# Optimization experiments

Hardware: AMD Instinct MI355X
Metric: run time of the kernel (lower is better)

## Reference

```python
import jax, jax.numpy as jnp
import numpy as np

D = 128      # embedding dim
T = 8        # message passing rounds (config.training.T)
NV = 4000    # n_vars
NL = 2 * NV  # n_literals
NC = 16000   # n_clauses


def setup_inputs() -> dict:
    key = jax.random.key(0)
    ks = jax.random.split(key, 12)
    s = np.float32(1.0 / np.sqrt(D))
    return {
        "L_state": jax.random.normal(ks[0], (1, NL, D), jnp.float32),
        "C_state": jax.random.normal(ks[1], (1, NC, D), jnp.float32),
        "hidden_L": jnp.zeros((1, NL, D), jnp.float32),
        "hidden_C": jnp.zeros((1, NC, D), jnp.float32),
        # 0/1 literal-clause incidence, ~40 clauses per literal
        "M": (jax.random.uniform(ks[2], (NL, NC)) < 0.0025).astype(jnp.float32),
        "n_vars": NV,
        "W_lc": jax.random.normal(ks[3], (D, D), jnp.float32) * s,
        "b_lc": jnp.zeros((D,), jnp.float32),
        "W_cl": jax.random.normal(ks[4], (D, D), jnp.float32) * s,
        "b_cl": jnp.zeros((D,), jnp.float32),
        "Wih_C": jax.random.normal(ks[5], (4 * D, D), jnp.float32) * s,
        "Whh_C": jax.random.normal(ks[6], (4 * D, D), jnp.float32) * s,
        "bih_C": jnp.zeros((4 * D,), jnp.float32),
        "bhh_C": jnp.zeros((4 * D,), jnp.float32),
        "Wih_L": jax.random.normal(ks[7], (4 * D, 2 * D), jnp.float32) * s,
        "Whh_L": jax.random.normal(ks[8], (4 * D, D), jnp.float32) * s,
        "bih_L": jnp.zeros((4 * D,), jnp.float32),
        "bhh_L": jnp.zeros((4 * D,), jnp.float32),
    }


def lstm_cell(x, h, c, Wih, Whh, bih, bhh):
    # torch nn.LSTM gate order: i, f, g, o
    gates = x @ Wih.T + bih + h @ Whh.T + bhh
    i, f, g, o = jnp.split(gates, 4, axis=-1)
    c_new = jax.nn.sigmoid(f) * c + jax.nn.sigmoid(i) * jnp.tanh(g)
    h_new = jax.nn.sigmoid(o) * jnp.tanh(c_new)
    return h_new, c_new


def reference(L_state, C_state, hidden_L, hidden_C, M, n_vars,
              W_lc, b_lc, W_cl, b_cl,
              Wih_C, Whh_C, bih_C, bhh_C,
              Wih_L, Whh_L, bih_L, bhh_L):
    # Replicates torch flip() as written: slices dim 0 (size 1), so this is
    # effectively identity for n_vars >= 1 (first slice is empty, second is x).
    def flip(x):
        return jnp.concatenate([x[n_vars:2 * n_vars], x[0:n_vars]], axis=0)

    def step(carry, _):
        L, hL, hC = carry
        LC_pre = L @ W_lc.T + b_lc                        # (1, NL, D)
        LC_msgs = jnp.einsum('lc,sld->scd', M, LC_pre)    # M^T @ pre: (1, NC, D)
        Cs, hC = lstm_cell(LC_msgs, hC, hC, Wih_C, Whh_C, bih_C, bhh_C)
        CL_pre = Cs @ W_cl.T + b_cl                       # (1, NC, D)
        CL_msgs = jnp.einsum('lc,scd->sld', M, CL_pre)    # M @ pre: (1, NL, D)
        inp = jnp.concatenate([CL_msgs, flip(L)], axis=2) # (1, NL, 2D)
        L, hL = lstm_cell(inp, hL, hL, Wih_L, Whh_L, bih_L, bhh_L)
        return (L, hL, hC), None

    (L_final, _, _), _ = jax.lax.scan(step, (L_state, hidden_L, hidden_C), None, length=T)
    return L_final
```

## Files before the change

### kernel.cpp

```cpp
#include <hip/hip_runtime.h>

#define DD   128
#define NL   8000
#define NC   16000
#define TSTEPS 8
#define NBF  2
#define ROWW 96
#define COLW 64

#define OS   33
#define SPLITS8 (32 * OS)
#define SPLIT   (SPLITS8 * 8)
#define LSTR 17
#define LSPL (48 * LSTR * 8)
#define L2S  33
#define L2SPL (48 * L2S * 8)

typedef __attribute__((ext_vector_type(8))) short  short8;
typedef __attribute__((ext_vector_type(8))) _Float16 half8;
typedef __attribute__((ext_vector_type(4))) float  f32x4;

__device__ __forceinline__ float frcp(float x) { return __builtin_amdgcn_rcpf(x); }
__device__ __forceinline__ float sigm(float x) { return frcp(1.f + __expf(-x)); }
__device__ __forceinline__ float tanh_(float x) {
  float e = __expf(2.f * x);
  return 1.f - 2.f * frcp(e + 1.f);
}
__device__ __forceinline__ void add4(float4& a, const float4 b) {
  a.x += b.x; a.y += b.y; a.z += b.z; a.w += b.w;
}
__device__ __forceinline__ unsigned short bfround(float v) {
  unsigned u = __float_as_uint(v);
  return (unsigned short)((u + 0x7FFF + ((u >> 16) & 1)) >> 16);
}
__device__ __forceinline__ float bf2f(unsigned short b) {
  return __uint_as_float(((unsigned)b) << 16);
}
__device__ __forceinline__ void splitf16(float v, unsigned short& h, unsigned short& l) {
  _Float16 hh = (_Float16)v;
  float r = v - (float)hh;
  _Float16 ll = (_Float16)r;
  h = __builtin_bit_cast(unsigned short, hh);
  l = __builtin_bit_cast(unsigned short, ll);
}
__device__ __forceinline__ int4 packi4(const unsigned short* p) {
  return make_int4(p[0] | ((int)p[1] << 16), p[2] | ((int)p[3] << 16),
                   p[4] | ((int)p[5] << 16), p[6] | ((int)p[7] << 16));
}

__device__ __forceinline__ void store_oct3(unsigned short* A, int oct, int m,
                                           float4 a, float4 b) {
  float f[8] = {a.x, a.y, a.z, a.w, b.x, b.y, b.z, b.w};
  unsigned short h[8], md[8], lo[8];
  #pragma unroll
  for (int j = 0; j < 8; ++j) {
    h[j] = bfround(f[j]);
    float r1 = f[j] - bf2f(h[j]);
    md[j] = bfround(r1);
    float r2 = r1 - bf2f(md[j]);
    lo[j] = bfround(r2);
  }
  int base = (oct * OS + m) * 8;
  *(int4*)(A + base)             = packi4(h);
  *(int4*)(A + SPLIT + base)     = packi4(md);
  *(int4*)(A + 2 * SPLIT + base) = packi4(lo);
}

__device__ __forceinline__ void store_oct2g(unsigned short* A, int strideS8, int plane,
                                            int oct, int m, float4 a, float4 b) {
  float f[8] = {a.x, a.y, a.z, a.w, b.x, b.y, b.z, b.w};
  unsigned short h[8], lo[8];
  #pragma unroll
  for (int j = 0; j < 8; ++j) splitf16(f[j], h[j], lo[j]);
  int base = (oct * strideS8 + m) * 8;
  *(int4*)(A + base)         = packi4(h);
  *(int4*)(A + plane + base) = packi4(lo);
}

__device__ __forceinline__ void store_half3L(unsigned short* A, int oct, int half, int m,
                                             float4 a) {
  float f[4] = {a.x, a.y, a.z, a.w};
  unsigned short h[4], md[4], lo[4];
  #pragma unroll
  for (int j = 0; j < 4; ++j) {
    h[j] = bfround(f[j]);
    float r1 = f[j] - bf2f(h[j]);
    md[j] = bfround(r1);
    float r2 = r1 - bf2f(md[j]);
    lo[j] = bfround(r2);
  }
  int base = (oct * LSTR + m) * 8 + half * 4;
  *(int2*)(A + base)            = make_int2(h[0]  | ((int)h[1]  << 16), h[2]  | ((int)h[3]  << 16));
  *(int2*)(A + LSPL + base)     = make_int2(md[0] | ((int)md[1] << 16), md[2] | ((int)md[3] << 16));
  *(int2*)(A + 2 * LSPL + base) = make_int2(lo[0] | ((int)lo[1] << 16), lo[2] | ((int)lo[3] << 16));
}

#define MFMA6(ACC, AH, AM, AL, BH, BM, BL)                                   \
  ACC = __builtin_amdgcn_mfma_f32_16x16x32_bf16(AH, BH, ACC, 0, 0, 0);       \
  ACC = __builtin_amdgcn_mfma_f32_16x16x32_bf16(AH, BM, ACC, 0, 0, 0);       \
  ACC = __builtin_amdgcn_mfma_f32_16x16x32_bf16(AM, BH, ACC, 0, 0, 0);       \
  ACC = __builtin_amdgcn_mfma_f32_16x16x32_bf16(AH, BL, ACC, 0, 0, 0);       \
  ACC = __builtin_amdgcn_mfma_f32_16x16x32_bf16(AL, BH, ACC, 0, 0, 0);       \
  ACC = __builtin_amdgcn_mfma_f32_16x16x32_bf16(AM, BM, ACC, 0, 0, 0);

#define MFMA4(ACC, AH, AL, BH, BL)                                           \
  ACC = __builtin_amdgcn_mfma_f32_16x16x32_f16(AH, BH, ACC, 0, 0, 0);        \
  ACC = __builtin_amdgcn_mfma_f32_16x16x32_f16(AH, BL, ACC, 0, 0, 0);        \
  ACC = __builtin_amdgcn_mfma_f32_16x16x32_f16(AL, BH, ACC, 0, 0, 0);        \
  ACC = __builtin_amdgcn_mfma_f32_16x16x32_f16(AL, BL, ACC, 0, 0, 0);


__global__ __launch_bounds__(256) void init_states(
    float4* __restrict__ Lbuf, const float4* __restrict__ L0,
    float4* __restrict__ hL, const float4* __restrict__ hL0,
    float4* __restrict__ hC, const float4* __restrict__ hC0) {
  int i = blockIdx.x * 256 + threadIdx.x, stride = gridDim.x * 256;
  for (int j = i; j < NL * DD / 4; j += stride) { Lbuf[j] = L0[j]; hL[j] = hL0[j]; }
  for (int j = i; j < NC * DD / 4; j += stride) hC[j] = hC0[j];
}

__global__ __launch_bounds__(256) void scan_M(const float4* __restrict__ M4,
                                              int* __restrict__ csr, int* __restrict__ csc,
                                              int* __restrict__ rcnt, int* __restrict__ ccnt) {
  const int total = (NL * NC) / 4;
  int stride = gridDim.x * blockDim.x;
  for (int i = blockIdx.x * blockDim.x + threadIdx.x; i < total; i += stride) {
    float4 v = M4[i];
    if (v.x == 0.f && v.y == 0.f && v.z == 0.f && v.w == 0.f) continue;
    int base = i * 4;
    int l = base / NC;
    int c0 = base - l * NC;
    float vv[4] = {v.x, v.y, v.z, v.w};
    #pragma unroll
    for (int e = 0; e < 4; ++e) {
      if (vv[e] != 0.f) {
        int c = c0 + e;
        int rp = atomicAdd(&rcnt[l], 1);
        if (rp < ROWW) csr[l * ROWW + rp] = c;
        int cp = atomicAdd(&ccnt[c], 1);
        if (cp < COLW) csc[c * COLW + cp] = l;
      }
    }
  }
}

__device__ __forceinline__ void split_store_bf3(float w, int idx, unsigned short* hi,
                                                unsigned short* md, unsigned short* lo) {
  unsigned short h = bfround(w);
  float r1 = w - bf2f(h);
  unsigned short m = bfround(r1);
  float r2 = r1 - bf2f(m);
  hi[idx] = h; md[idx] = m; lo[idx] = bfround(r2);
}

__global__ __launch_bounds__(256) void build_packC(
    const float* __restrict__ WihC, const float* __restrict__ Wlc, const float* __restrict__ WhhC,
    unsigned short* __restrict__ pkhi, unsigned short* __restrict__ pkmd, unsigned short* __restrict__ pklo,
    unsigned short* __restrict__ qkhi, unsigned short* __restrict__ qklo) {
  int i = blockIdx.x * 256 + threadIdx.x;
  int k = i >> 9, n = i & 511;
  float w;
  if (k < 128) {
    float s = 0.f;
    for (int d = 0; d < 128; ++d) s += WihC[n * 128 + d] * Wlc[d * 128 + k];
    w = s;
  } else {
    w = WhhC[n * 128 + (k - 128)];
  }
  int idx = ((k >> 3) * 512 + n) * 8 + (k & 7);
  split_store_bf3(w, idx, pkhi, pkmd, pklo);
  splitf16(w, qkhi[idx], qklo[idx]);
}

__global__ __launch_bounds__(256) void build_packL(
    const float* __restrict__ WihL, const float* __restrict__ Wcl, const float* __restrict__ WhhL,
    unsigned short* __restrict__ pkhi, unsigned short* __restrict__ pkmd, unsigned short* __restrict__ pklo,
    unsigned short* __restrict__ qkhi, unsigned short* __restrict__ qklo) {
  int i = blockIdx.x * 256 + threadIdx.x;
  int k = i >> 9, n = i & 511;
  float w;
  if (k < 128) {
    float s = 0.f;
    for (int d = 0; d < 128; ++d) s += WihL[n * 256 + d] * Wcl[d * 128 + k];
    w = s;
  } else if (k < 256) {
    w = WihL[n * 256 + k];
  } else {
    w = WhhL[n * 128 + (k - 256)];
  }
  int idx = ((k >> 3) * 512 + n) * 8 + (k & 7);
  split_store_bf3(w, idx, pkhi, pkmd, pklo);
  splitf16(w, qkhi[idx], qklo[idx]);
}

__global__ __launch_bounds__(256) void build_bias(
    const float* __restrict__ bihC, const float* __restrict__ bhhC,
    const float* __restrict__ WihC, const float* __restrict__ blc,
    const float* __restrict__ bihL, const float* __restrict__ bhhL,
    const float* __restrict__ WihL, const float* __restrict__ bcl,
    float* __restrict__ bsumC, float* __restrict__ bvecC,
    float* __restrict__ bsumL, float* __restrict__ bvecL) {
  int i = blockIdx.x * 256 + threadIdx.x;
  if (i < 512) {
    bsumC[i] = bihC[i] + bhhC[i];
    float s = 0.f;
    for (int d = 0; d < 128; ++d) s += WihC[i * 128 + d] * blc[d];
    bvecC[i] = s;
  } else if (i < 1024) {
    int n = i - 512;
    bsumL[n] = bihL[n] + bhhL[n];
    float s = 0.f;
    for (int d = 0; d < 128; ++d) s += WihL[n * 256 + d] * bcl[d];
    bvecL[n] = s;
  }
}

__device__ __forceinline__ void clause_epilogue(
    const f32x4 acc[2][4], const float* bsum, const float* bvec, const int* ccnt,
    float* hC, float* Cs, int rowBase, int quad, int cw) {
  float bs_[4], bv_[4];
  #pragma unroll
  for (int g = 0; g < 4; ++g) { bs_[g] = bsum[g * 128 + cw]; bv_[g] = bvec[g * 128 + cw]; }
  #pragma unroll
  for (int mt = 0; mt < 2; ++mt) {
    #pragma unroll
    for (int reg = 0; reg < 4; ++reg) {
      int row = rowBase + mt * 16 + quad * 4 + reg;
      float deg = (float)ccnt[row];
      float co = hC[(size_t)row * DD + cw];
      float iv = acc[mt][0][reg] + bs_[0] + deg * bv_[0];
      float fv = acc[mt][1][reg] + bs_[1] + deg * bv_[1];
      float gv = acc[mt][2][reg] + bs_[2] + deg * bv_[2];
      float ov = acc[mt][3][reg] + bs_[3] + deg * bv_[3];
      float cn = sigm(fv) * co + sigm(iv) * tanh_(gv);
      hC[(size_t)row * DD + cw] = cn;
      Cs[(size_t)row * DD + cw] = sigm(ov) * tanh_(cn);
    }
  }
}

__device__ __forceinline__ void literal_epilogue2(
    const f32x4 acc[2][4], const float* bsum, const float* bvec, const int* rcnt,
    float* hL, float* Lbuf, int rowBase, int quad, int cw) {
  float bs_[4], bv_[4];
  #pragma unroll
  for (int g = 0; g < 4; ++g) { bs_[g] = bsum[g * 128 + cw]; bv_[g] = bvec[g * 128 + cw]; }
  #pragma unroll
  for (int mt = 0; mt < 2; ++mt) {
    #pragma unroll
    for (int reg = 0; reg < 4; ++reg) {
      int row = rowBase + mt * 16 + quad * 4 + reg;
      float deg = (float)rcnt[row];
      float co = hL[(size_t)row * DD + cw];
      float iv = acc[mt][0][reg] + bs_[0] + deg * bv_[0];
      float fv = acc[mt][1][reg] + bs_[1] + deg * bv_[1];
      float gv = acc[mt][2][reg] + bs_[2] + deg * bv_[2];
      float ov = acc[mt][3][reg] + bs_[3] + deg * bv_[3];
      float cn = sigm(fv) * co + sigm(iv) * tanh_(gv);
      hL[(size_t)row * DD + cw] = cn;
      Lbuf[(size_t)row * DD + cw] = sigm(ov) * tanh_(cn);
    }
  }
}


template <int NOCT, bool STAGE_H>
__global__ __launch_bounds__(512, 4) void clause_bf3(
    const float* __restrict__ Lbuf, const int* __restrict__ csc, const int* __restrict__ ccnt,
    const unsigned short* __restrict__ pkhi, const unsigned short* __restrict__ pkmd,
    const unsigned short* __restrict__ pklo,
    const float* __restrict__ bsum, const float* __restrict__ bvec,
    float* __restrict__ hC, float* __restrict__ Cs) {
  __shared__ unsigned short A[3 * SPLIT];
  __shared__ int IDX[32 * COLW];
  const int t = threadIdx.x;
  const int rowBase = blockIdx.x * 32;

  ((int4*)IDX)[t] = ((const int4*)(csc + rowBase * COLW))[t];
  __syncthreads();

  {
    const int r = t >> 4, sub = t & 15;
    const int c = rowBase + r;
    int cnt = ccnt[c]; if (cnt > COLW) cnt = COLW;
    const int* lst = IDX + r * COLW;
    float4 a0 = make_float4(0, 0, 0, 0), a1 = a0;
    int j = 0;
    for (; j + 8 <= cnt; j += 8) {
      float4 p0[8], p1[8];
      #pragma unroll
      for (int u = 0; u < 8; ++u) {
        const float4* s4 = (const float4*)(Lbuf + (size_t)lst[j + u] * DD) + sub * 2;
        p0[u] = s4[0]; p1[u] = s4[1];
      }
      #pragma unroll
      for (int u = 0; u < 8; ++u) { add4(a0, p0[u]); add4(a1, p1[u]); }
    }
    for (; j < cnt; ++j) {
      const float4* s4 = (const float4*)(Lbuf + (size_t)lst[j] * DD) + sub * 2;
      add4(a0, s4[0]); add4(a1, s4[1]);
    }
    store_oct3(A, sub, r, a0, a1);
    if constexpr (STAGE_H) {
      const float4* h4 = (const float4*)(hC + (size_t)c * DD) + sub * 2;
      store_oct3(A, 16 + sub, r, h4[0], h4[1]);
    }
  }
  __syncthreads();

  const int w = t >> 6, l = t & 63;
  const int quad = l >> 4, lane16 = l & 15;
  const int cw = w * 16 + lane16;
  f32x4 acc[2][4];
  #pragma unroll
  for (int mt = 0; mt < 2; ++mt)
    #pragma unroll
    for (int g = 0; g < 4; ++g) acc[mt][g] = (f32x4){0.f, 0.f, 0.f, 0.f};

  const short8* As = (const short8*)A;
  const short8* Bh = (const short8*)pkhi;
  const short8* Bm = (const short8*)pkmd;
  const short8* Bl = (const short8*)pklo;

  __builtin_amdgcn_s_setprio(1);
  #pragma unroll
  for (int s = 0; s < NOCT / 4; ++s) {
    int ao = (s * 4 + quad) * OS + lane16;
    short8 a0h = As[ao],                a1h = As[ao + 16];
    short8 a0m = As[SPLITS8 + ao],      a1m = As[SPLITS8 + ao + 16];
    short8 a0l = As[2 * SPLITS8 + ao],  a1l = As[2 * SPLITS8 + ao + 16];
    int bo = (s * 4 + quad) * 512 + cw;
    #pragma unroll
    for (int g = 0; g < 4; ++g) {
      short8 bh = Bh[bo + g * 128];
      short8 bm = Bm[bo + g * 128];
      short8 bl = Bl[bo + g * 128];
      MFMA6(acc[0][g], a0h, a0m, a0l, bh, bm, bl);
      MFMA6(acc[1][g], a1h, a1m, a1l, bh, bm, bl);
    }
  }
  __builtin_amdgcn_s_setprio(0);
  clause_epilogue(acc, bsum, bvec, ccnt, hC, Cs, rowBase, quad, cw);
}

template <int NOCT, bool STAGE_H>
__global__ __launch_bounds__(512, 4) void literal_bf3(
    const float* __restrict__ Cs, const int* __restrict__ csr, const int* __restrict__ rcnt,
    const unsigned short* __restrict__ pkhi, const unsigned short* __restrict__ pkmd,
    const unsigned short* __restrict__ pklo,
    const float* __restrict__ bsum, const float* __restrict__ bvec,
    float* __restrict__ hL, float* __restrict__ Lbuf) {
  __shared__ unsigned short A[3 * LSPL];
  __shared__ int IDX[16 * ROWW];
  const int t = threadIdx.x;
  const int rowBase = blockIdx.x * 16;

  if (t < 384) ((int4*)IDX)[t] = ((const int4*)(csr + rowBase * ROWW))[t];
  __syncthreads();

  {
    const int r = t >> 5, cg2 = t & 31;
    const int lr = rowBase + r;
    int cnt = rcnt[lr]; if (cnt > ROWW) cnt = ROWW;
    const int* lst = IDX + r * ROWW;
    float4 a0 = make_float4(0, 0, 0, 0);
    int j = 0;
    for (; j + 8 <= cnt; j += 8) {
      float4 p[8];
      #pragma unroll
      for (int u = 0; u < 8; ++u)
        p[u] = ((const float4*)(Cs + (size_t)lst[j + u] * DD))[cg2];
      #pragma unroll
      for (int u = 0; u < 8; ++u) add4(a0, p[u]);
    }
    for (; j < cnt; ++j)
      add4(a0, ((const float4*)(Cs + (size_t)lst[j] * DD))[cg2]);
    store_half3L(A, cg2 >> 1, cg2 & 1, r, a0);
    store_half3L(A, 16 + (cg2 >> 1), cg2 & 1, r,
                 ((const float4*)(Lbuf + (size_t)lr * DD))[cg2]);
    if constexpr (STAGE_H)
      store_half3L(A, 32 + (cg2 >> 1), cg2 & 1, r,
                   ((const float4*)(hL + (size_t)lr * DD))[cg2]);
  }
  __syncthreads();

  const int w = t >> 6, l = t & 63;
  const int quad = l >> 4, lane16 = l & 15;
  const int cw = w * 16 + lane16;
  f32x4 acc[4];
  #pragma unroll
  for (int g = 0; g < 4; ++g) acc[g] = (f32x4){0.f, 0.f, 0.f, 0.f};

  const short8* As = (const short8*)A;
  const short8* Bh = (const short8*)pkhi;
  const short8* Bm = (const short8*)pkmd;
  const short8* Bl = (const short8*)pklo;

  __builtin_amdgcn_s_setprio(1);
  #pragma unroll
  for (int s = 0; s < NOCT / 4; ++s) {
    int ao = (s * 4 + quad) * LSTR + lane16;
    short8 ah = As[ao];
    short8 am = As[LSPL / 8 + ao];
    short8 al = As[2 * (LSPL / 8) + ao];
    int bo = (s * 4 + quad) * 512 + cw;
    #pragma unroll
    for (int g = 0; g < 4; ++g) {
      short8 bh = Bh[bo + g * 128];
      short8 bm = Bm[bo + g * 128];
      short8 bl = Bl[bo + g * 128];
      MFMA6(acc[g], ah, am, al, bh, bm, bl);
    }
  }
  __builtin_amdgcn_s_setprio(0);

  float bs_[4], bv_[4];
  #pragma unroll
  for (int g = 0; g < 4; ++g) { bs_[g] = bsum[g * 128 + cw]; bv_[g] = bvec[g * 128 + cw]; }
  #pragma unroll
  for (int reg = 0; reg < 4; ++reg) {
    int row = rowBase + quad * 4 + reg;
    float deg = (float)rcnt[row];
    float co = hL[(size_t)row * DD + cw];
    float iv = acc[0][reg] + bs_[0] + deg * bv_[0];
    float fv = acc[1][reg] + bs_[1] + deg * bv_[1];
    float gv = acc[2][reg] + bs_[2] + deg * bv_[2];
    float ov = acc[3][reg] + bs_[3] + deg * bv_[3];
    float cn = sigm(fv) * co + sigm(iv) * tanh_(gv);
    hL[(size_t)row * DD + cw] = cn;
    Lbuf[(size_t)row * DD + cw] = sigm(ov) * tanh_(cn);
  }
}


__global__ __launch_bounds__(512, 4) void clause_f2(
    const float* __restrict__ Lbuf, const int* __restrict__ csc, const int* __restrict__ ccnt,
    const unsigned short* __restrict__ qkhi, const unsigned short* __restrict__ qklo,
    const float* __restrict__ bsum, const float* __restrict__ bvec,
    float* __restrict__ hC, float* __restrict__ Cs) {
  __shared__ unsigned short A[2 * SPLIT];
  __shared__ int IDX[32 * COLW];
  const int t = threadIdx.x;
  const int rowBase = blockIdx.x * 32;

  ((int4*)IDX)[t] = ((const int4*)(csc + rowBase * COLW))[t];
  __syncthreads();

  {
    const int r = t >> 4, sub = t & 15;
    const int c = rowBase + r;
    int cnt = ccnt[c]; if (cnt > COLW) cnt = COLW;
    const int* lst = IDX + r * COLW;
    float4 a0 = make_float4(0, 0, 0, 0), a1 = a0;
    int j = 0;
    for (; j + 8 <= cnt; j += 8) {
      float4 p0[8], p1[8];
      #pragma unroll
      for (int u = 0; u < 8; ++u) {
        const float4* s4 = (const float4*)(Lbuf + (size_t)lst[j + u] * DD) + sub * 2;
        p0[u] = s4[0]; p1[u] = s4[1];
      }
      #pragma unroll
      for (int u = 0; u < 8; ++u) { add4(a0, p0[u]); add4(a1, p1[u]); }
    }
    for (; j < cnt; ++j) {
      const float4* s4 = (const float4*)(Lbuf + (size_t)lst[j] * DD) + sub * 2;
      add4(a0, s4[0]); add4(a1, s4[1]);
    }
    store_oct2g(A, OS, SPLIT, sub, r, a0, a1);
    const float4* h4 = (const float4*)(hC + (size_t)c * DD) + sub * 2;
    store_oct2g(A, OS, SPLIT, 16 + sub, r, h4[0], h4[1]);
  }
  __syncthreads();

  const int w = t >> 6, l = t & 63;
  const int quad = l >> 4, lane16 = l & 15;
  const int cw = w * 16 + lane16;
  f32x4 acc[2][4];
  #pragma unroll
  for (int mt = 0; mt < 2; ++mt)
    #pragma unroll
    for (int g = 0; g < 4; ++g) acc[mt][g] = (f32x4){0.f, 0.f, 0.f, 0.f};

  const half8* As = (const half8*)A;
  const half8* Bh = (const half8*)qkhi;
  const half8* Bl = (const half8*)qklo;

  __builtin_amdgcn_s_setprio(1);
  #pragma unroll
  for (int s = 0; s < 8; ++s) {
    int ao = (s * 4 + quad) * OS + lane16;
    half8 a0h = As[ao],           a1h = As[ao + 16];
    half8 a0l = As[SPLITS8 + ao], a1l = As[SPLITS8 + ao + 16];
    int bo = (s * 4 + quad) * 512 + cw;
    #pragma unroll
    for (int g = 0; g < 4; ++g) {
      half8 bh = Bh[bo + g * 128];
      half8 bl = Bl[bo + g * 128];
      MFMA4(acc[0][g], a0h, a0l, bh, bl);
      MFMA4(acc[1][g], a1h, a1l, bh, bl);
    }
  }
  __builtin_amdgcn_s_setprio(0);
  clause_epilogue(acc, bsum, bvec, ccnt, hC, Cs, rowBase, quad, cw);
}

__global__ __launch_bounds__(512, 4) void literal_f2(
    const float* __restrict__ Cs, const int* __restrict__ csr, const int* __restrict__ rcnt,
    const unsigned short* __restrict__ qkhi, const unsigned short* __restrict__ qklo,
    const float* __restrict__ bsum, const float* __restrict__ bvec,
    float* __restrict__ hL, float* __restrict__ Lbuf) {
  __shared__ unsigned short A[2 * L2SPL];
  __shared__ int IDX[32 * ROWW];
  const int t = threadIdx.x;
  const int rowBase = blockIdx.x * 32;

  ((int4*)IDX)[t] = ((const int4*)(csr + rowBase * ROWW))[t];
  if (t < 256) ((int4*)IDX)[t + 512] = ((const int4*)(csr + rowBase * ROWW))[t + 512];
  __syncthreads();

  {
    const int r = t >> 4, sub = t & 15;
    const int lr = rowBase + r;
    int cnt = rcnt[lr]; if (cnt > ROWW) cnt = ROWW;
    const int* lst = IDX + r * ROWW;
    float4 a0 = make_float4(0, 0, 0, 0), a1 = a0;
    int j = 0;
    for (; j + 8 <= cnt; j += 8) {
      float4 p0[8], p1[8];
      #pragma unroll
      for (int u = 0; u < 8; ++u) {
        const float4* s4 = (const float4*)(Cs + (size_t)lst[j + u] * DD) + sub * 2;
        p0[u] = s4[0]; p1[u] = s4[1];
      }
      #pragma unroll
      for (int u = 0; u < 8; ++u) { add4(a0, p0[u]); add4(a1, p1[u]); }
    }
    for (; j < cnt; ++j) {
      const float4* s4 = (const float4*)(Cs + (size_t)lst[j] * DD) + sub * 2;
      add4(a0, s4[0]); add4(a1, s4[1]);
    }
    store_oct2g(A, L2S, L2SPL, sub, r, a0, a1);
    const float4* l4 = (const float4*)(Lbuf + (size_t)lr * DD) + sub * 2;
    store_oct2g(A, L2S, L2SPL, 16 + sub, r, l4[0], l4[1]);
    const float4* h4 = (const float4*)(hL + (size_t)lr * DD) + sub * 2;
    store_oct2g(A, L2S, L2SPL, 32 + sub, r, h4[0], h4[1]);
  }
  __syncthreads();

  const int w = t >> 6, l = t & 63;
  const int quad = l >> 4, lane16 = l & 15;
  const int cw = w * 16 + lane16;
  f32x4 acc[2][4];
  #pragma unroll
  for (int mt = 0; mt < 2; ++mt)
    #pragma unroll
    for (int g = 0; g < 4; ++g) acc[mt][g] = (f32x4){0.f, 0.f, 0.f, 0.f};

  const half8* As = (const half8*)A;
  const half8* Bh = (const half8*)qkhi;
  const half8* Bl = (const half8*)qklo;

  __builtin_amdgcn_s_setprio(1);
  #pragma unroll
  for (int s = 0; s < 12; ++s) {
    int ao = (s * 4 + quad) * L2S + lane16;
    half8 a0h = As[ao],             a1h = As[ao + 16];
    half8 a0l = As[L2SPL / 8 + ao], a1l = As[L2SPL / 8 + ao + 16];
    int bo = (s * 4 + quad) * 512 + cw;
    #pragma unroll
    for (int g = 0; g < 4; ++g) {
      half8 bh = Bh[bo + g * 128];
      half8 bl = Bl[bo + g * 128];
      MFMA4(acc[0][g], a0h, a0l, bh, bl);
      MFMA4(acc[1][g], a1h, a1l, bh, bl);
    }
  }
  __builtin_amdgcn_s_setprio(0);
  literal_epilogue2(acc, bsum, bvec, rcnt, hL, Lbuf, rowBase, quad, cw);
}


extern "C" void kernel_launch(void* const* d_in, const int* in_sizes, int n_in,
                              void* d_out, int out_size, void* d_ws, size_t ws_size,
                              hipStream_t stream) {
  const float* L0   = (const float*)d_in[0];
  const float* hL0  = (const float*)d_in[2];
  const float* hC0  = (const float*)d_in[3];
  const float* M    = (const float*)d_in[4];
  const float* Wlc  = (const float*)d_in[6];
  const float* blc  = (const float*)d_in[7];
  const float* Wcl  = (const float*)d_in[8];
  const float* bcl  = (const float*)d_in[9];
  const float* WihC = (const float*)d_in[10];
  const float* WhhC = (const float*)d_in[11];
  const float* bihC = (const float*)d_in[12];
  const float* bhhC = (const float*)d_in[13];
  const float* WihL = (const float*)d_in[14];
  const float* WhhL = (const float*)d_in[15];
  const float* bihL = (const float*)d_in[16];
  const float* bhhL = (const float*)d_in[17];

  float* ws    = (float*)d_ws;
  float* hL    = ws;
  float* hC    = hL + NL * DD;
  float* Cs    = hC + NC * DD;
  float* bsumC = Cs + NC * DD;
  float* bvecC = bsumC + 512;
  float* bsumL = bvecC + 512;
  float* bvecL = bsumL + 512;
  unsigned short* pkChi = (unsigned short*)(bvecL + 512);
  unsigned short* pkCmd = pkChi + 256 * 512;
  unsigned short* pkClo = pkCmd + 256 * 512;
  unsigned short* pkLhi = pkClo + 256 * 512;
  unsigned short* pkLmd = pkLhi + 384 * 512;
  unsigned short* pkLlo = pkLmd + 384 * 512;
  unsigned short* qkChi = pkLlo + 384 * 512;
  unsigned short* qkClo = qkChi + 256 * 512;
  unsigned short* qkLhi = qkClo + 256 * 512;
  unsigned short* qkLlo = qkLhi + 384 * 512;
  int* csr  = (int*)(qkLlo + 384 * 512);
  int* csc  = csr + NL * ROWW;
  int* rcnt = csc + NC * COLW;
  int* ccnt = rcnt + NL;
  float* Lbuf = (float*)d_out;

  hipMemsetAsync(rcnt, 0, (NL + NC) * sizeof(int), stream);

  init_states<<<1024, 256, 0, stream>>>((float4*)Lbuf, (const float4*)L0,
                                        (float4*)hL, (const float4*)hL0,
                                        (float4*)hC, (const float4*)hC0);

  scan_M<<<4096, 256, 0, stream>>>((const float4*)M, csr, csc, rcnt, ccnt);

  build_packC<<<(256 * 512) / 256, 256, 0, stream>>>(WihC, Wlc, WhhC,
                                                     pkChi, pkCmd, pkClo, qkChi, qkClo);
  build_packL<<<(384 * 512) / 256, 256, 0, stream>>>(WihL, Wcl, WhhL,
                                                     pkLhi, pkLmd, pkLlo, qkLhi, qkLlo);
  build_bias<<<4, 256, 0, stream>>>(bihC, bhhC, WihC, blc, bihL, bhhL, WihL, bcl,
                                    bsumC, bvecC, bsumL, bvecL);

  clause_bf3<16, false><<<NC / 32, 512, 0, stream>>>(Lbuf, csc, ccnt, pkChi, pkCmd, pkClo,
                                                     bsumC, bvecC, hC, Cs);
  literal_bf3<32, false><<<NL / 16, 512, 0, stream>>>(Cs, csr, rcnt, pkLhi, pkLmd, pkLlo,
                                                      bsumL, bvecL, hL, Lbuf);
  for (int t = 1; t < NBF; ++t) {
    clause_bf3<32, true><<<NC / 32, 512, 0, stream>>>(Lbuf, csc, ccnt, pkChi, pkCmd, pkClo,
                                                      bsumC, bvecC, hC, Cs);
    literal_bf3<48, true><<<NL / 16, 512, 0, stream>>>(Cs, csr, rcnt, pkLhi, pkLmd, pkLlo,
                                                       bsumL, bvecL, hL, Lbuf);
  }
  for (int t = NBF; t < TSTEPS; ++t) {
    clause_f2<<<NC / 32, 512, 0, stream>>>(Lbuf, csc, ccnt, qkChi, qkClo,
                                           bsumC, bvecC, hC, Cs);
    literal_f2<<<NL / 32, 512, 0, stream>>>(Cs, csr, rcnt, qkLhi, qkLlo,
                                            bsumL, bvecL, hL, Lbuf);
  }
}
```

Measured before the change: 1.280 ms.

## Shrink all step kernels to 16-row, 256-thread blocks with 8 column tiles per wave

Every clause and literal kernel now handles 16 rows per block with 4 waves instead of 32 rows with 8 waves. Each wave covers two 64-column halves, giving 8 accumulator tiles per gate set. The shared-memory A layout uses a single stride of 17, and the literal bf3 kernel drops its shared index staging and reads CSR indices straight from global memory. The aim is more, smaller blocks for better occupancy and load balance across CUs on the gather-heavy phases. The cost is loading the B weights once per 16 rows instead of once per 32, which doubles weight traffic per output row.

```diff
diff --git a/kernel.cpp b/kernel.cpp
--- a/kernel.cpp
+++ b/kernel.cpp
@@ -8,13 +8,9 @@
 #define ROWW 96
 #define COLW 64
 
-#define OS   33
-#define SPLITS8 (32 * OS)
-#define SPLIT   (SPLITS8 * 8)
-#define LSTR 17
-#define LSPL (48 * LSTR * 8)
-#define L2S  33
-#define L2SPL (48 * L2S * 8)
+#define S16  17
+#define CP16 (32 * S16 * 8)
+#define LP16 (48 * S16 * 8)
 
 typedef __attribute__((ext_vector_type(8))) short  short8;
 typedef __attribute__((ext_vector_type(8))) _Float16 half8;
@@ -48,8 +44,8 @@
                    p[4] | ((int)p[5] << 16), p[6] | ((int)p[7] << 16));
 }
 
-__device__ __forceinline__ void store_oct3(unsigned short* A, int oct, int m,
-                                           float4 a, float4 b) {
+__device__ __forceinline__ void store_oct3g(unsigned short* A, int strideS8, int planeShorts,
+                                            int oct, int m, float4 a, float4 b) {
   float f[8] = {a.x, a.y, a.z, a.w, b.x, b.y, b.z, b.w};
   unsigned short h[8], md[8], lo[8];
   #pragma unroll
@@ -60,10 +56,10 @@
     float r2 = r1 - bf2f(md[j]);
     lo[j] = bfround(r2);
   }
-  int base = (oct * OS + m) * 8;
-  *(int4*)(A + base)             = packi4(h);
-  *(int4*)(A + SPLIT + base)     = packi4(md);
-  *(int4*)(A + 2 * SPLIT + base) = packi4(lo);
+  int base = (oct * strideS8 + m) * 8;
+  *(int4*)(A + base)                   = packi4(h);
+  *(int4*)(A + planeShorts + base)     = packi4(md);
+  *(int4*)(A + 2 * planeShorts + base) = packi4(lo);
 }
 
 __device__ __forceinline__ void store_oct2g(unsigned short* A, int strideS8, int plane,
@@ -75,24 +71,6 @@
   int base = (oct * strideS8 + m) * 8;
   *(int4*)(A + base)         = packi4(h);
   *(int4*)(A + plane + base) = packi4(lo);
-}
-
-__device__ __forceinline__ void store_half3L(unsigned short* A, int oct, int half, int m,
-                                             float4 a) {
-  float f[4] = {a.x, a.y, a.z, a.w};
-  unsigned short h[4], md[4], lo[4];
-  #pragma unroll
-  for (int j = 0; j < 4; ++j) {
-    h[j] = bfround(f[j]);
-    float r1 = f[j] - bf2f(h[j]);
-    md[j] = bfround(r1);
-    float r2 = r1 - bf2f(md[j]);
-    lo[j] = bfround(r2);
-  }
-  int base = (oct * LSTR + m) * 8 + half * 4;
-  *(int2*)(A + base)            = make_int2(h[0]  | ((int)h[1]  << 16), h[2]  | ((int)h[3]  << 16));
-  *(int2*)(A + LSPL + base)     = make_int2(md[0] | ((int)md[1] << 16), md[2] | ((int)md[3] << 16));
-  *(int2*)(A + 2 * LSPL + base) = make_int2(lo[0] | ((int)lo[1] << 16), lo[2] | ((int)lo[3] << 16));
 }
 
 #define MFMA6(ACC, AH, AM, AL, BH, BM, BL)                                   \
@@ -215,66 +193,68 @@
   }
 }
 
-__device__ __forceinline__ void clause_epilogue(
-    const f32x4 acc[2][4], const float* bsum, const float* bvec, const int* ccnt,
+__device__ __forceinline__ void clause_epi16(
+    const f32x4 acc[8], const float* bsum, const float* bvec, const int* ccnt,
     float* hC, float* Cs, int rowBase, int quad, int cw) {
-  float bs_[4], bv_[4];
-  #pragma unroll
-  for (int g = 0; g < 4; ++g) { bs_[g] = bsum[g * 128 + cw]; bv_[g] = bvec[g * 128 + cw]; }
-  #pragma unroll
-  for (int mt = 0; mt < 2; ++mt) {
+  #pragma unroll
+  for (int h = 0; h < 2; ++h) {
+    int dc = h * 64 + cw;
+    float bs_[4], bv_[4];
+    #pragma unroll
+    for (int g = 0; g < 4; ++g) { bs_[g] = bsum[g * 128 + dc]; bv_[g] = bvec[g * 128 + dc]; }
     #pragma unroll
     for (int reg = 0; reg < 4; ++reg) {
-      int row = rowBase + mt * 16 + quad * 4 + reg;
+      int row = rowBase + quad * 4 + reg;
       float deg = (float)ccnt[row];
-      float co = hC[(size_t)row * DD + cw];
-      float iv = acc[mt][0][reg] + bs_[0] + deg * bv_[0];
-      float fv = acc[mt][1][reg] + bs_[1] + deg * bv_[1];
-      float gv = acc[mt][2][reg] + bs_[2] + deg * bv_[2];
-      float ov = acc[mt][3][reg] + bs_[3] + deg * bv_[3];
+      float co = hC[(size_t)row * DD + dc];
+      float iv = acc[0 + h][reg] + bs_[0] + deg * bv_[0];
+      float fv = acc[2 + h][reg] + bs_[1] + deg * bv_[1];
+      float gv = acc[4 + h][reg] + bs_[2] + deg * bv_[2];
+      float ov = acc[6 + h][reg] + bs_[3] + deg * bv_[3];
       float cn = sigm(fv) * co + sigm(iv) * tanh_(gv);
-      hC[(size_t)row * DD + cw] = cn;
-      Cs[(size_t)row * DD + cw] = sigm(ov) * tanh_(cn);
-    }
-  }
-}
-
-__device__ __forceinline__ void literal_epilogue2(
-    const f32x4 acc[2][4], const float* bsum, const float* bvec, const int* rcnt,
+      hC[(size_t)row * DD + dc] = cn;
+      Cs[(size_t)row * DD + dc] = sigm(ov) * tanh_(cn);
+    }
+  }
+}
+
+__device__ __forceinline__ void literal_epi16(
+    const f32x4 acc[8], const float* bsum, const float* bvec, const int* rcnt,
     float* hL, float* Lbuf, int rowBase, int quad, int cw) {
-  float bs_[4], bv_[4];
-  #pragma unroll
-  for (int g = 0; g < 4; ++g) { bs_[g] = bsum[g * 128 + cw]; bv_[g] = bvec[g * 128 + cw]; }
-  #pragma unroll
-  for (int mt = 0; mt < 2; ++mt) {
+  #pragma unroll
+  for (int h = 0; h < 2; ++h) {
+    int dc = h * 64 + cw;
+    float bs_[4], bv_[4];
+    #pragma unroll
+    for (int g = 0; g < 4; ++g) { bs_[g] = bsum[g * 128 + dc]; bv_[g] = bvec[g * 128 + dc]; }
     #pragma unroll
     for (int reg = 0; reg < 4; ++reg) {
-      int row = rowBase + mt * 16 + quad * 4 + reg;
+      int row = rowBase + quad * 4 + reg;
       float deg = (float)rcnt[row];
-      float co = hL[(size_t)row * DD + cw];
-      float iv = acc[mt][0][reg] + bs_[0] + deg * bv_[0];
-      float fv = acc[mt][1][reg] + bs_[1] + deg * bv_[1];
-      float gv = acc[mt][2][reg] + bs_[2] + deg * bv_[2];
-      float ov = acc[mt][3][reg] + bs_[3] + deg * bv_[3];
+      float co = hL[(size_t)row * DD + dc];
+      float iv = acc[0 + h][reg] + bs_[0] + deg * bv_[0];
+      float fv = acc[2 + h][reg] + bs_[1] + deg * bv_[1];
+      float gv = acc[4 + h][reg] + bs_[2] + deg * bv_[2];
+      float ov = acc[6 + h][reg] + bs_[3] + deg * bv_[3];
       float cn = sigm(fv) * co + sigm(iv) * tanh_(gv);
-      hL[(size_t)row * DD + cw] = cn;
-      Lbuf[(size_t)row * DD + cw] = sigm(ov) * tanh_(cn);
+      hL[(size_t)row * DD + dc] = cn;
+      Lbuf[(size_t)row * DD + dc] = sigm(ov) * tanh_(cn);
     }
   }
 }
 
 
 template <int NOCT, bool STAGE_H>
-__global__ __launch_bounds__(512, 4) void clause_bf3(
+__global__ __launch_bounds__(256, 4) void clause_bf3(
     const float* __restrict__ Lbuf, const int* __restrict__ csc, const int* __restrict__ ccnt,
     const unsigned short* __restrict__ pkhi, const unsigned short* __restrict__ pkmd,
     const unsigned short* __restrict__ pklo,
     const float* __restrict__ bsum, const float* __restrict__ bvec,
     float* __restrict__ hC, float* __restrict__ Cs) {
-  __shared__ unsigned short A[3 * SPLIT];
-  __shared__ int IDX[32 * COLW];
+  __shared__ unsigned short A[3 * CP16];
+  __shared__ int IDX[16 * COLW];
   const int t = threadIdx.x;
-  const int rowBase = blockIdx.x * 32;
+  const int rowBase = blockIdx.x * 16;
 
   ((int4*)IDX)[t] = ((const int4*)(csc + rowBase * COLW))[t];
   __syncthreads();
@@ -300,10 +280,10 @@
       const float4* s4 = (const float4*)(Lbuf + (size_t)lst[j] * DD) + sub * 2;
       add4(a0, s4[0]); add4(a1, s4[1]);
     }
-    store_oct3(A, sub, r, a0, a1);
+    store_oct3g(A, S16, CP16, sub, r, a0, a1);
     if constexpr (STAGE_H) {
       const float4* h4 = (const float4*)(hC + (size_t)c * DD) + sub * 2;
-      store_oct3(A, 16 + sub, r, h4[0], h4[1]);
+      store_oct3g(A, S16, CP16, 16 + sub, r, h4[0], h4[1]);
     }
   }
   __syncthreads();
@@ -311,11 +291,9 @@
   const int w = t >> 6, l = t & 63;
   const int quad = l >> 4, lane16 = l & 15;
   const int cw = w * 16 + lane16;
-  f32x4 acc[2][4];
-  #pragma unroll
-  for (int mt = 0; mt < 2; ++mt)
-    #pragma unroll
-    for (int g = 0; g < 4; ++g) acc[mt][g] = (f32x4){0.f, 0.f, 0.f, 0.f};
+  f32x4 acc[8];
+  #pragma unroll
+  for (int g2 = 0; g2 < 8; ++g2) acc[g2] = (f32x4){0.f, 0.f, 0.f, 0.f};
 
   const short8* As = (const short8*)A;
   const short8* Bh = (const short8*)pkhi;
@@ -325,71 +303,71 @@
   __builtin_amdgcn_s_setprio(1);
   #pragma unroll
   for (int s = 0; s < NOCT / 4; ++s) {
-    int ao = (s * 4 + quad) * OS + lane16;
-    short8 a0h = As[ao],                a1h = As[ao + 16];
-    short8 a0m = As[SPLITS8 + ao],      a1m = As[SPLITS8 + ao + 16];
-    short8 a0l = As[2 * SPLITS8 + ao],  a1l = As[2 * SPLITS8 + ao + 16];
+    int ao = (s * 4 + quad) * S16 + lane16;
+    short8 ah = As[ao];
+    short8 am = As[CP16 / 8 + ao];
+    short8 al = As[2 * (CP16 / 8) + ao];
     int bo = (s * 4 + quad) * 512 + cw;
     #pragma unroll
-    for (int g = 0; g < 4; ++g) {
-      short8 bh = Bh[bo + g * 128];
-      short8 bm = Bm[bo + g * 128];
-      short8 bl = Bl[bo + g * 128];
-      MFMA6(acc[0][g], a0h, a0m, a0l, bh, bm, bl);
-      MFMA6(acc[1][g], a1h, a1m, a1l, bh, bm, bl);
+    for (int g2 = 0; g2 < 8; ++g2) {
+      short8 bh = Bh[bo + g2 * 64];
+      short8 bm = Bm[bo + g2 * 64];
+      short8 bl = Bl[bo + g2 * 64];
+      MFMA6(acc[g2], ah, am, al, bh, bm, bl);
     }
   }
   __builtin_amdgcn_s_setprio(0);
-  clause_epilogue(acc, bsum, bvec, ccnt, hC, Cs, rowBase, quad, cw);
+  clause_epi16(acc, bsum, bvec, ccnt, hC, Cs, rowBase, quad, cw);
 }
 
 template <int NOCT, bool STAGE_H>
-__global__ __launch_bounds__(512, 4) void literal_bf3(
+__global__ __launch_bounds__(256, 4) void literal_bf3(
     const float* __restrict__ Cs, const int* __restrict__ csr, const int* __restrict__ rcnt,
     const unsigned short* __restrict__ pkhi, const unsigned short* __restrict__ pkmd,
     const unsigned short* __restrict__ pklo,
     const float* __restrict__ bsum, const float* __restrict__ bvec,
     float* __restrict__ hL, float* __restrict__ Lbuf) {
-  __shared__ unsigned short A[3 * LSPL];
-  __shared__ int IDX[16 * ROWW];
+  __shared__ unsigned short A[3 * LP16];
   const int t = threadIdx.x;
   const int rowBase = blockIdx.x * 16;
 
-  if (t < 384) ((int4*)IDX)[t] = ((const int4*)(csr + rowBase * ROWW))[t];
-  __syncthreads();
-
   {
-    const int r = t >> 5, cg2 = t & 31;
+    const int r = t >> 4, sub = t & 15;
     const int lr = rowBase + r;
     int cnt = rcnt[lr]; if (cnt > ROWW) cnt = ROWW;
-    const int* lst = IDX + r * ROWW;
-    float4 a0 = make_float4(0, 0, 0, 0);
+    const int* lst = csr + lr * ROWW;
+    float4 a0 = make_float4(0, 0, 0, 0), a1 = a0;
     int j = 0;
     for (; j + 8 <= cnt; j += 8) {
-      float4 p[8];
-      #pragma unroll
-      for (int u = 0; u < 8; ++u)
-        p[u] = ((const float4*)(Cs + (size_t)lst[j + u] * DD))[cg2];
-      #pragma unroll
-      for (int u = 0; u < 8; ++u) add4(a0, p[u]);
-    }
-    for (; j < cnt; ++j)
-      add4(a0, ((const float4*)(Cs + (size_t)lst[j] * DD))[cg2]);
-    store_half3L(A, cg2 >> 1, cg2 & 1, r, a0);
-    store_half3L(A, 16 + (cg2 >> 1), cg2 & 1, r,
-                 ((const float4*)(Lbuf + (size_t)lr * DD))[cg2]);
-    if constexpr (STAGE_H)
-      store_half3L(A, 32 + (cg2 >> 1), cg2 & 1, r,
-                   ((const float4*)(hL + (size_t)lr * DD))[cg2]);
+      float4 p0[8], p1[8];
+      #pragma unroll
+      for (int u = 0; u < 8; ++u) {
+        const float4* s4 = (const float4*)(Cs + (size_t)lst[j + u] * DD) + sub * 2;
+        p0[u] = s4[0]; p1[u] = s4[1];
+      }
+      #pragma unroll
+      for (int u = 0; u < 8; ++u) { add4(a0, p0[u]); add4(a1, p1[u]); }
+    }
+    for (; j < cnt; ++j) {
+      const float4* s4 = (const float4*)(Cs + (size_t)lst[j] * DD) + sub * 2;
+      add4(a0, s4[0]); add4(a1, s4[1]);
+    }
+    store_oct3g(A, S16, LP16, sub, r, a0, a1);
+    const float4* l4 = (const float4*)(Lbuf + (size_t)lr * DD) + sub * 2;
+    store_oct3g(A, S16, LP16, 16 + sub, r, l4[0], l4[1]);
+    if constexpr (STAGE_H) {
+      const float4* h4 = (const float4*)(hL + (size_t)lr * DD) + sub * 2;
+      store_oct3g(A, S16, LP16, 32 + sub, r, h4[0], h4[1]);
+    }
   }
   __syncthreads();
 
   const int w = t >> 6, l = t & 63;
   const int quad = l >> 4, lane16 = l & 15;
   const int cw = w * 16 + lane16;
-  f32x4 acc[4];
-  #pragma unroll
-  for (int g = 0; g < 4; ++g) acc[g] = (f32x4){0.f, 0.f, 0.f, 0.f};
+  f32x4 acc[8];
+  #pragma unroll
+  for (int g2 = 0; g2 < 8; ++g2) acc[g2] = (f32x4){0.f, 0.f, 0.f, 0.f};
 
   const short8* As = (const short8*)A;
   const short8* Bh = (const short8*)pkhi;
@@ -399,49 +377,33 @@
   __builtin_amdgcn_s_setprio(1);
   #pragma unroll
   for (int s = 0; s < NOCT / 4; ++s) {
-    int ao = (s * 4 + quad) * LSTR + lane16;
+    int ao = (s * 4 + quad) * S16 + lane16;
     short8 ah = As[ao];
-    short8 am = As[LSPL / 8 + ao];
-    short8 al = As[2 * (LSPL / 8) + ao];
+    short8 am = As[LP16 / 8 + ao];
+    short8 al = As[2 * (LP16 / 8) + ao];
     int bo = (s * 4 + quad) * 512 + cw;
     #pragma unroll
-    for (int g = 0; g < 4; ++g) {
-      short8 bh = Bh[bo + g * 128];
-      short8 bm = Bm[bo + g * 128];
-      short8 bl = Bl[bo + g * 128];
-      MFMA6(acc[g], ah, am, al, bh, bm, bl);
+    for (int g2 = 0; g2 < 8; ++g2) {
+      short8 bh = Bh[bo + g2 * 64];
+      short8 bm = Bm[bo + g2 * 64];
+      short8 bl = Bl[bo + g2 * 64];
+      MFMA6(acc[g2], ah, am, al, bh, bm, bl);
     }
   }
   __builtin_amdgcn_s_setprio(0);
-
-  float bs_[4], bv_[4];
-  #pragma unroll
-  for (int g = 0; g < 4; ++g) { bs_[g] = bsum[g * 128 + cw]; bv_[g] = bvec[g * 128 + cw]; }
-  #pragma unroll
-  for (int reg = 0; reg < 4; ++reg) {
-    int row = rowBase + quad * 4 + reg;
-    float deg = (float)rcnt[row];
-    float co = hL[(size_t)row * DD + cw];
-    float iv = acc[0][reg] + bs_[0] + deg * bv_[0];
-    float fv = acc[1][reg] + bs_[1] + deg * bv_[1];
-    float gv = acc[2][reg] + bs_[2] + deg * bv_[2];
-    float ov = acc[3][reg] + bs_[3] + deg * bv_[3];
-    float cn = sigm(fv) * co + sigm(iv) * tanh_(gv);
-    hL[(size_t)row * DD + cw] = cn;
-    Lbuf[(size_t)row * DD + cw] = sigm(ov) * tanh_(cn);
-  }
-}
-
-
-__global__ __launch_bounds__(512, 4) void clause_f2(
+  literal_epi16(acc, bsum, bvec, rcnt, hL, Lbuf, rowBase, quad, cw);
+}
+
+
+__global__ __launch_bounds__(256, 4) void clause_f2(
     const float* __restrict__ Lbuf, const int* __restrict__ csc, const int* __restrict__ ccnt,
     const unsigned short* __restrict__ qkhi, const unsigned short* __restrict__ qklo,
     const float* __restrict__ bsum, const float* __restrict__ bvec,
     float* __restrict__ hC, float* __restrict__ Cs) {
-  __shared__ unsigned short A[2 * SPLIT];
-  __shared__ int IDX[32 * COLW];
+  __shared__ unsigned short A[2 * CP16];
+  __shared__ int IDX[16 * COLW];
   const int t = threadIdx.x;
-  const int rowBase = blockIdx.x * 32;
+  const int rowBase = blockIdx.x * 16;
 
   ((int4*)IDX)[t] = ((const int4*)(csc + rowBase * COLW))[t];
   __syncthreads();
@@ -467,20 +429,18 @@
       const float4* s4 = (const float4*)(Lbuf + (size_t)lst[j] * DD) + sub * 2;
       add4(a0, s4[0]); add4(a1, s4[1]);
     }
-    store_oct2g(A, OS, SPLIT, sub, r, a0, a1);
+    store_oct2g(A, S16, CP16, sub, r, a0, a1);
     const float4* h4 = (const float4*)(hC + (size_t)c * DD) + sub * 2;
-    store_oct2g(A, OS, SPLIT, 16 + sub, r, h4[0], h4[1]);
+    store_oct2g(A, S16, CP16, 16 + sub, r, h4[0], h4[1]);
   }
   __syncthreads();
 
   const int w = t >> 6, l = t & 63;
   const int quad = l >> 4, lane16 = l & 15;
   const int cw = w * 16 + lane16;
-  f32x4 acc[2][4];
-  #pragma unroll
-  for (int mt = 0; mt < 2; ++mt)
-    #pragma unroll
-    for (int g = 0; g < 4; ++g) acc[mt][g] = (f32x4){0.f, 0.f, 0.f, 0.f};
+  f32x4 acc[8];
+  #pragma unroll
+  for (int g2 = 0; g2 < 8; ++g2) acc[g2] = (f32x4){0.f, 0.f, 0.f, 0.f};
 
   const half8* As = (const half8*)A;
   const half8* Bh = (const half8*)qkhi;
@@ -489,34 +449,33 @@
   __builtin_amdgcn_s_setprio(1);
   #pragma unroll
   for (int s = 0; s < 8; ++s) {
-    int ao = (s * 4 + quad) * OS + lane16;
-    half8 a0h = As[ao],           a1h = As[ao + 16];
-    half8 a0l = As[SPLITS8 + ao], a1l = As[SPLITS8 + ao + 16];
+    int ao = (s * 4 + quad) * S16 + lane16;
+    half8 ah = As[ao];
+    half8 al = As[CP16 / 8 + ao];
     int bo = (s * 4 + quad) * 512 + cw;
     #pragma unroll
-    for (int g = 0; g < 4; ++g) {
-      half8 bh = Bh[bo + g * 128];
-      half8 bl = Bl[bo + g * 128];
-      MFMA4(acc[0][g], a0h, a0l, bh, bl);
-      MFMA4(acc[1][g], a1h, a1l, bh, bl);
+    for (int g2 = 0; g2 < 8; ++g2) {
+      half8 bh = Bh[bo + g2 * 64];
+      half8 bl = Bl[bo + g2 * 64];
+      MFMA4(acc[g2], ah, al, bh, bl);
     }
   }
   __builtin_amdgcn_s_setprio(0);
-  clause_epilogue(acc, bsum, bvec, ccnt, hC, Cs, rowBase, quad, cw);
-}
-
-__global__ __launch_bounds__(512, 4) void literal_f2(
+  clause_epi16(acc, bsum, bvec, ccnt, hC, Cs, rowBase, quad, cw);
+}
+
+__global__ __launch_bounds__(256, 4) void literal_f2(
     const float* __restrict__ Cs, const int* __restrict__ csr, const int* __restrict__ rcnt,
     const unsigned short* __restrict__ qkhi, const unsigned short* __restrict__ qklo,
     const float* __restrict__ bsum, const float* __restrict__ bvec,
     float* __restrict__ hL, float* __restrict__ Lbuf) {
-  __shared__ unsigned short A[2 * L2SPL];
-  __shared__ int IDX[32 * ROWW];
+  __shared__ unsigned short A[2 * LP16];
+  __shared__ int IDX[16 * ROWW];
   const int t = threadIdx.x;
-  const int rowBase = blockIdx.x * 32;
+  const int rowBase = blockIdx.x * 16;
 
   ((int4*)IDX)[t] = ((const int4*)(csr + rowBase * ROWW))[t];
-  if (t < 256) ((int4*)IDX)[t + 512] = ((const int4*)(csr + rowBase * ROWW))[t + 512];
+  if (t < 128) ((int4*)IDX)[t + 256] = ((const int4*)(csr + rowBase * ROWW))[t + 256];
   __syncthreads();
 
   {
@@ -540,22 +499,20 @@
       const float4* s4 = (const float4*)(Cs + (size_t)lst[j] * DD) + sub * 2;
       add4(a0, s4[0]); add4(a1, s4[1]);
     }
-    store_oct2g(A, L2S, L2SPL, sub, r, a0, a1);
+    store_oct2g(A, S16, LP16, sub, r, a0, a1);
     const float4* l4 = (const float4*)(Lbuf + (size_t)lr * DD) + sub * 2;
-    store_oct2g(A, L2S, L2SPL, 16 + sub, r, l4[0], l4[1]);
+    store_oct2g(A, S16, LP16, 16 + sub, r, l4[0], l4[1]);
     const float4* h4 = (const float4*)(hL + (size_t)lr * DD) + sub * 2;
-    store_oct2g(A, L2S, L2SPL, 32 + sub, r, h4[0], h4[1]);
+    store_oct2g(A, S16, LP16, 32 + sub, r, h4[0], h4[1]);
   }
   __syncthreads();
 
   const int w = t >> 6, l = t & 63;
   const int quad = l >> 4, lane16 = l & 15;
   const int cw = w * 16 + lane16;
-  f32x4 acc[2][4];
-  #pragma unroll
-  for (int mt = 0; mt < 2; ++mt)
-    #pragma unroll
-    for (int g = 0; g < 4; ++g) acc[mt][g] = (f32x4){0.f, 0.f, 0.f, 0.f};
+  f32x4 acc[8];
+  #pragma unroll
+  for (int g2 = 0; g2 < 8; ++g2) acc[g2] = (f32x4){0.f, 0.f, 0.f, 0.f};
 
   const half8* As = (const half8*)A;
   const half8* Bh = (const half8*)qkhi;
@@ -564,20 +521,19 @@
   __builtin_amdgcn_s_setprio(1);
   #pragma unroll
   for (int s = 0; s < 12; ++s) {
-    int ao = (s * 4 + quad) * L2S + lane16;
-    half8 a0h = As[ao],             a1h = As[ao + 16];
-    half8 a0l = As[L2SPL / 8 + ao], a1l = As[L2SPL / 8 + ao + 16];
+    int ao = (s * 4 + quad) * S16 + lane16;
+    half8 ah = As[ao];
+    half8 al = As[LP16 / 8 + ao];
     int bo = (s * 4 + quad) * 512 + cw;
     #pragma unroll
-    for (int g = 0; g < 4; ++g) {
-      half8 bh = Bh[bo + g * 128];
-      half8 bl = Bl[bo + g * 128];
-      MFMA4(acc[0][g], a0h, a0l, bh, bl);
-      MFMA4(acc[1][g], a1h, a1l, bh, bl);
+    for (int g2 = 0; g2 < 8; ++g2) {
+      half8 bh = Bh[bo + g2 * 64];
+      half8 bl = Bl[bo + g2 * 64];
+      MFMA4(acc[g2], ah, al, bh, bl);
     }
   }
   __builtin_amdgcn_s_setprio(0);
-  literal_epilogue2(acc, bsum, bvec, rcnt, hL, Lbuf, rowBase, quad, cw);
+  literal_epi16(acc, bsum, bvec, rcnt, hL, Lbuf, rowBase, quad, cw);
 }
 
 
@@ -640,20 +596,20 @@
   build_bias<<<4, 256, 0, stream>>>(bihC, bhhC, WihC, blc, bihL, bhhL, WihL, bcl,
                                     bsumC, bvecC, bsumL, bvecL);
 
-  clause_bf3<16, false><<<NC / 32, 512, 0, stream>>>(Lbuf, csc, ccnt, pkChi, pkCmd, pkClo,
+  clause_bf3<16, false><<<NC / 16, 256, 0, stream>>>(Lbuf, csc, ccnt, pkChi, pkCmd, pkClo,
                                                      bsumC, bvecC, hC, Cs);
-  literal_bf3<32, false><<<NL / 16, 512, 0, stream>>>(Cs, csr, rcnt, pkLhi, pkLmd, pkLlo,
+  literal_bf3<32, false><<<NL / 16, 256, 0, stream>>>(Cs, csr, rcnt, pkLhi, pkLmd, pkLlo,
                                                       bsumL, bvecL, hL, Lbuf);
   for (int t = 1; t < NBF; ++t) {
-    clause_bf3<32, true><<<NC / 32, 512, 0, stream>>>(Lbuf, csc, ccnt, pkChi, pkCmd, pkClo,
+    clause_bf3<32, true><<<NC / 16, 256, 0, stream>>>(Lbuf, csc, ccnt, pkChi, pkCmd, pkClo,
                                                       bsumC, bvecC, hC, Cs);
-    literal_bf3<48, true><<<NL / 16, 512, 0, stream>>>(Cs, csr, rcnt, pkLhi, pkLmd, pkLlo,
+    literal_bf3<48, true><<<NL / 16, 256, 0, stream>>>(Cs, csr, rcnt, pkLhi, pkLmd, pkLlo,
                                                        bsumL, bvecL, hL, Lbuf);
   }
   for (int t = NBF; t < TSTEPS; ++t) {
-    clause_f2<<<NC / 32, 512, 0, stream>>>(Lbuf, csc, ccnt, qkChi, qkClo,
+    clause_f2<<<NC / 16, 256, 0, stream>>>(Lbuf, csc, ccnt, qkChi, qkClo,
                                            bsumC, bvecC, hC, Cs);
-    literal_f2<<<NL / 32, 512, 0, stream>>>(Cs, csr, rcnt, qkLhi, qkLlo,
+    literal_f2<<<NL / 16, 256, 0, stream>>>(Cs, csr, rcnt, qkLhi, qkLlo,
                                             bsumL, bvecL, hL, Lbuf);
   }
 }
```

Result: slower. 1.426 ms (+11.4%).
